# Optimization experiments

Hardware: AMD Instinct MI355X
Metric: run time of the kernel (lower is better)

The kernel has to match this reference:

```python
import jax, jax.numpy as jnp
import numpy as np

D, H, W, C = 24, 24, 16, 2        # image_dims + num_classes
THETA_ALPHA = 160.0               # bilateral spatial std
THETA_BETA = 3.0                  # bilateral intensity std
THETA_GAMMA = 3.0                 # spatial-only std
NUM_ITERATIONS = 5
N = D * H * W


def _gauss_kernel(feats):
    # Dense Gaussian kernel K_ij = exp(-0.5 * ||f_i - f_j||^2).
    # This is the exact filter that the permutohedral lattice approximates
    # (self-term included, matching the lattice splat/blur/slice behaviour).
    sq = jnp.sum(feats * feats, axis=-1)               # [N]
    d2 = sq[:, None] + sq[None, :] - 2.0 * feats @ feats.T
    return jnp.exp(-0.5 * jnp.maximum(d2, 0.0))        # [N, N]


def _positions():
    zz, yy, xx = jnp.meshgrid(jnp.arange(D), jnp.arange(H), jnp.arange(W), indexing='ij')
    return jnp.stack([zz, yy, xx], axis=-1).reshape(N, 3).astype(jnp.float32)


def setup_inputs() -> dict:
    key = jax.random.key(0)
    k1, k2 = jax.random.split(key)
    unaries = jax.random.normal(k1, (1, D, H, W, C), dtype=jnp.float32)
    rgb = jax.random.uniform(k2, (1, D, H, W, 1), dtype=jnp.float32)
    # learned params (build() initial values)
    spatial_ker_weights = jnp.array([1.41, 1.41], dtype=jnp.float32)
    bilateral_ker_weights = jnp.array([3.85, 3.85], dtype=jnp.float32)
    compatibility_matrix = jnp.eye(C, dtype=jnp.float32)
    return dict(unaries=unaries, rgb=rgb,
                spatial_ker_weights=spatial_ker_weights,
                bilateral_ker_weights=bilateral_ker_weights,
                compatibility_matrix=compatibility_matrix)


def reference(unaries, rgb, spatial_ker_weights, bilateral_ker_weights, compatibility_matrix):
    out_shape = unaries.shape
    u = unaries.reshape(N, C)                 # batch index 0 only, as in the TF code
    img = rgb.reshape(N, -1)
    pos = _positions()

    Ks = _gauss_kernel(pos / THETA_GAMMA)                                        # spatial kernel [N,N]
    Kb = _gauss_kernel(jnp.concatenate([pos / THETA_ALPHA, img / THETA_BETA], -1))  # bilateral kernel [N,N]

    # normalization = filter applied to all-ones (row sums)
    norm_s = jnp.sum(Ks, axis=-1, keepdims=True)   # [N,1]
    norm_b = jnp.sum(Kb, axis=-1, keepdims=True)   # [N,1]

    q = u
    for _ in range(NUM_ITERATIONS):
        spatial_out = (Ks @ q) / norm_s            # [N,C]
        bilateral_out = (Kb @ q) / norm_b          # [N,C]
        # diag(w_s) @ spatial.T + diag(w_b) @ bilateral.T  ==  per-class scaling
        message = spatial_out * spatial_ker_weights + bilateral_out * bilateral_ker_weights
        pairwise = message @ compatibility_matrix.T  # (compat @ msg.T).T
        q = u - pairwise
    return q.reshape(out_shape)
```

## Files before the change

### kernel.cpp

```cpp
#include <hip/hip_runtime.h>


#define DD 24
#define HH 24
#define WW 16
#define SLICE 384
#define NPTS 9216
#define NT 5
#define NPAIR 6
#define NPTOT 9
#define LOG2E 1.4426950408889634f
#define K3L   (LOG2E / 18.0f)
#define K160L (LOG2E / 51200.0f)
#define EXP2  __builtin_amdgcn_exp2f

static __device__ __forceinline__ int iabs(int a) { return a < 0 ? -a : a; }

__global__ __launch_bounds__(SLICE)
void k_pre(const float2* __restrict__ u2, const float* __restrict__ rgb,
           float2* __restrict__ tmp2, float* __restrict__ normS) {
    __shared__ float gk[32];
    __shared__ float2 sA[HH][WW + 1];
    __shared__ float2 sB[HH][WW + 1];
    const int z = blockIdx.x, p = blockIdx.y, t = threadIdx.x;
    const int y = t >> 4, x = t & 15;
    const int i = z * SLICE + t;

    const float kk = (p == 0) ? K3L : K160L;
    if (t < DD) gk[t] = EXP2(-(float)(t * t) * kk);

    const float I3 = rgb[i] * (1.f / 3.f);
    float Pt[NT];
    Pt[0] = EXP2(-0.5f * LOG2E * I3 * I3);
#pragma unroll
    for (int k = 1; k < NT; ++k) Pt[k] = Pt[k - 1] * I3;

    float2 v;
    if (p == 0) {
        v = u2[i];
    } else if (p < NPAIR) {
        float2 q = u2[i];
        float P = Pt[p - 1];
        v = make_float2(P * q.x, P * q.y);
    } else {
        int j = p - NPAIR;
        v = make_float2(Pt[2 * j], (j < 2) ? Pt[2 * j + 1] : 0.f);
    }
    sA[y][x] = v;
    __syncthreads();

    float a0 = 0.f, a1 = 0.f;
#pragma unroll
    for (int xp = 0; xp < WW; ++xp) {
        float w = gk[iabs(x - xp)];
        float2 vv = sA[y][xp];
        a0 = fmaf(w, vv.x, a0);
        a1 = fmaf(w, vv.y, a1);
    }
    sB[y][x] = make_float2(a0, a1);
    __syncthreads();
    float b0 = 0.f, b1 = 0.f;
#pragma unroll
    for (int yp = 0; yp < HH; ++yp) {
        float w = gk[iabs(y - yp)];
        float2 vv = sB[yp][x];
        b0 = fmaf(w, vv.x, b0);
        b1 = fmaf(w, vv.y, b1);
    }
    tmp2[p * NPTS + i] = make_float2(b0, b1);

    if (p == 0) {
        float sx = 0.f, sy = 0.f, sz = 0.f;
#pragma unroll
        for (int xp = 0; xp < WW; ++xp) sx += gk[iabs(x - xp)];
#pragma unroll
        for (int yp = 0; yp < HH; ++yp) sy += gk[iabs(y - yp)];
#pragma unroll
        for (int zp = 0; zp < DD; ++zp) sz += gk[iabs(z - zp)];
        normS[i] = 1.0f / (sx * sy * sz);
    }
}

__global__ __launch_bounds__(SLICE)
void k_zconv(const float2* __restrict__ tmp2, float2* __restrict__ zout2) {
    const int z = blockIdx.x, p = blockIdx.y, t = threadIdx.x;
    const float kk = (p == 0) ? K3L : K160L;
    float acc0 = 0.f, acc1 = 0.f;
    const float2* src = tmp2 + p * NPTS + t;
#pragma unroll 6
    for (int zp = 0; zp < DD; ++zp) {
        int d = z - zp;
        float w = EXP2(-(float)(d * d) * kk);
        float2 v = src[zp * SLICE];
        acc0 = fmaf(w, v.x, acc0);
        acc1 = fmaf(w, v.y, acc1);
    }
    zout2[p * NPTS + z * SLICE + t] = make_float2(acc0, acc1);
}

static __device__ __forceinline__ void mf_update(
        const float2 zp_[NPAIR], const float* Pt, float inv_ns, float inv_nb,
        const float* sw, const float* bw, const float* compat,
        const float2 uu, float* q0o, float* q1o) {
    const float invf[NT] = {1.f, 1.f, 0.5f, 1.f / 6.f, 1.f / 24.f};
    float b0 = 0.f, b1 = 0.f;
#pragma unroll
    for (int k = 0; k < NT; ++k) {
        float w = Pt[k] * invf[k];
        b0 = fmaf(w, zp_[1 + k].x, b0);
        b1 = fmaf(w, zp_[1 + k].y, b1);
    }
    b0 *= inv_nb;
    b1 *= inv_nb;
    float s0 = zp_[0].x * inv_ns;
    float s1 = zp_[0].y * inv_ns;
    float m0 = s0 * sw[0] + b0 * bw[0];
    float m1 = s1 * sw[1] + b1 * bw[1];
    float p0 = fmaf(compat[0], m0, compat[1] * m1);
    float p1 = fmaf(compat[2], m0, compat[3] * m1);
    *q0o = uu.x - p0;
    *q1o = uu.y - p1;
}

__global__ __launch_bounds__(SLICE)
void k_xyupd(const float2* __restrict__ zout2, const float* __restrict__ rgb,
             const float2* __restrict__ u2,
             const float* __restrict__ sw, const float* __restrict__ bw,
             const float* __restrict__ compat,
             const float* __restrict__ normS, float* __restrict__ normB,
             float2* __restrict__ tmp2, int it) {
    __shared__ float gk[32];
    __shared__ float2 sA[HH][WW + 1];
    __shared__ float2 sB[HH][WW + 1];
    const int z = blockIdx.x, p = blockIdx.y, t = threadIdx.x;
    const int y = t >> 4, x = t & 15;
    const int i = z * SLICE + t;

    const float kk = (p == 0) ? K3L : K160L;
    if (t < DD) gk[t] = EXP2(-(float)(t * t) * kk);

    float2 zp_[NPAIR];
#pragma unroll
    for (int k = 0; k < NPAIR; ++k) zp_[k] = zout2[k * NPTS + i];

    const float I3 = rgb[i] * (1.f / 3.f);
    float Pt[NT];
    Pt[0] = EXP2(-0.5f * LOG2E * I3 * I3);
#pragma unroll
    for (int k = 1; k < NT; ++k) Pt[k] = Pt[k - 1] * I3;

    float inv_nb;
    if (it == 0) {
        float2 n0 = zout2[6 * NPTS + i];
        float2 n1 = zout2[7 * NPTS + i];
        float2 n2 = zout2[8 * NPTS + i];
        float nb = Pt[0] * n0.x + Pt[1] * n0.y + 0.5f * Pt[2] * n1.x
                 + (1.f / 6.f) * Pt[3] * n1.y + (1.f / 24.f) * Pt[4] * n2.x;
        if (p == 0) normB[i] = nb;
        inv_nb = 1.0f / nb;
    } else {
        inv_nb = 1.0f / normB[i];
    }

    float q0, q1;
    mf_update(zp_, Pt, normS[i], inv_nb, sw, bw, compat, u2[i], &q0, &q1);

    float2 v;
    if (p == 0) v = make_float2(q0, q1);
    else { float P = Pt[p - 1]; v = make_float2(P * q0, P * q1); }

    sA[y][x] = v;
    __syncthreads();
    float a0 = 0.f, a1 = 0.f;
#pragma unroll
    for (int xp = 0; xp < WW; ++xp) {
        float w = gk[iabs(x - xp)];
        float2 vv = sA[y][xp];
        a0 = fmaf(w, vv.x, a0);
        a1 = fmaf(w, vv.y, a1);
    }
    sB[y][x] = make_float2(a0, a1);
    __syncthreads();
    float b0 = 0.f, b1 = 0.f;
#pragma unroll
    for (int yp = 0; yp < HH; ++yp) {
        float w = gk[iabs(y - yp)];
        float2 vv = sB[yp][x];
        b0 = fmaf(w, vv.x, b0);
        b1 = fmaf(w, vv.y, b1);
    }
    tmp2[p * NPTS + i] = make_float2(b0, b1);
}

__global__ __launch_bounds__(256)
void k_final(const float2* __restrict__ zout2, const float* __restrict__ rgb,
             const float2* __restrict__ u2,
             const float* __restrict__ sw, const float* __restrict__ bw,
             const float* __restrict__ compat,
             const float* __restrict__ normS, const float* __restrict__ normB,
             float2* __restrict__ out) {
    const int i = blockIdx.x * 256 + threadIdx.x;

    float2 zp_[NPAIR];
#pragma unroll
    for (int k = 0; k < NPAIR; ++k) zp_[k] = zout2[k * NPTS + i];

    const float I3 = rgb[i] * (1.f / 3.f);
    float Pt[NT];
    Pt[0] = EXP2(-0.5f * LOG2E * I3 * I3);
#pragma unroll
    for (int k = 1; k < NT; ++k) Pt[k] = Pt[k - 1] * I3;

    float q0, q1;
    mf_update(zp_, Pt, normS[i], 1.0f / normB[i], sw, bw, compat,
              u2[i], &q0, &q1);
    out[i] = make_float2(q0, q1);
}

extern "C" void kernel_launch(void* const* d_in, const int* in_sizes, int n_in,
                              void* d_out, int out_size, void* d_ws, size_t ws_size,
                              hipStream_t stream) {
    const float2* u2     = (const float2*)d_in[0];
    const float*  rgb    = (const float*)d_in[1];
    const float*  sw     = (const float*)d_in[2];
    const float*  bw     = (const float*)d_in[3];
    const float*  compat = (const float*)d_in[4];
    float2* out = (float2*)d_out;

    float2* ws2   = (float2*)d_ws;
    float2* tmp2  = ws2;
    float2* zout2 = ws2 + NPTOT * NPTS;
    float*  normS = (float*)(ws2 + 2 * NPTOT * NPTS);
    float*  normB = normS + NPTS;

    k_pre<<<dim3(DD, NPTOT), SLICE, 0, stream>>>(u2, rgb, tmp2, normS);

    for (int it = 0; it < 5; ++it) {
        k_zconv<<<dim3(DD, it == 0 ? NPTOT : NPAIR), SLICE, 0, stream>>>(tmp2, zout2);
        if (it < 4)
            k_xyupd<<<dim3(DD, NPAIR), SLICE, 0, stream>>>(zout2, rgb, u2, sw, bw,
                                                           compat, normS, normB,
                                                           tmp2, it);
        else
            k_final<<<NPTS / 256, 256, 0, stream>>>(zout2, rgb, u2, sw, bw,
                                                    compat, normS, normB, out);
    }
}
```

Baseline: 97.28 us.

## Fuse all CRF stages into one persistent kernel with global barriers

```diff
diff --git a/kernel.cpp b/kernel.cpp
--- a/kernel.cpp
+++ b/kernel.cpp
@@ -8,7 +8,7 @@
 #define NPTS 9216
 #define NT 5
 #define NPAIR 6
-#define NPTOT 9
+#define NB (DD * NPAIR)
 #define LOG2E 1.4426950408889634f
 #define K3L   (LOG2E / 18.0f)
 #define K160L (LOG2E / 51200.0f)
@@ -16,39 +16,42 @@
 
 static __device__ __forceinline__ int iabs(int a) { return a < 0 ? -a : a; }
 
-__global__ __launch_bounds__(SLICE)
-void k_pre(const float2* __restrict__ u2, const float* __restrict__ rgb,
-           float2* __restrict__ tmp2, float* __restrict__ normS) {
-    __shared__ float gk[32];
-    __shared__ float2 sA[HH][WW + 1];
-    __shared__ float2 sB[HH][WW + 1];
-    const int z = blockIdx.x, p = blockIdx.y, t = threadIdx.x;
-    const int y = t >> 4, x = t & 15;
-    const int i = z * SLICE + t;
-
-    const float kk = (p == 0) ? K3L : K160L;
-    if (t < DD) gk[t] = EXP2(-(float)(t * t) * kk);
-
-    const float I3 = rgb[i] * (1.f / 3.f);
-    float Pt[NT];
-    Pt[0] = EXP2(-0.5f * LOG2E * I3 * I3);
-#pragma unroll
-    for (int k = 1; k < NT; ++k) Pt[k] = Pt[k - 1] * I3;
-
-    float2 v;
-    if (p == 0) {
-        v = u2[i];
-    } else if (p < NPAIR) {
-        float2 q = u2[i];
-        float P = Pt[p - 1];
-        v = make_float2(P * q.x, P * q.y);
-    } else {
-        int j = p - NPAIR;
-        v = make_float2(Pt[2 * j], (j < 2) ? Pt[2 * j + 1] : 0.f);
-    }
+static __device__ __forceinline__ float2 ldc2(const float2* p) {
+    unsigned long long v = __hip_atomic_load((unsigned long long*)p,
+                               __ATOMIC_RELAXED, __HIP_MEMORY_SCOPE_AGENT);
+    float2 f;
+    __builtin_memcpy(&f, &v, 8);
+    return f;
+}
+static __device__ __forceinline__ void stc2(float2* p, float2 f) {
+    unsigned long long v;
+    __builtin_memcpy(&v, &f, 8);
+    __hip_atomic_store((unsigned long long*)p, v,
+                       __ATOMIC_RELAXED, __HIP_MEMORY_SCOPE_AGENT);
+}
+
+static __device__ __forceinline__ void gbar(unsigned* bar, int ph) {
+    __syncthreads();
+    if (threadIdx.x == 0) {
+        __builtin_amdgcn_s_waitcnt(0);
+        __hip_atomic_fetch_add(&bar[ph], 1u, __ATOMIC_RELAXED,
+                               __HIP_MEMORY_SCOPE_AGENT);
+        while (__hip_atomic_load(&bar[ph], __ATOMIC_RELAXED,
+                                 __HIP_MEMORY_SCOPE_AGENT) < (unsigned)NB)
+            __builtin_amdgcn_s_sleep(2);
+    }
+    __syncthreads();
+}
+
+__global__ void k_init(unsigned* bar) {
+    if (threadIdx.x < 16) bar[threadIdx.x] = 0u;
+}
+
+static __device__ void xyconv(float2 v, int y, int x, const float* gk,
+                              float2 (*sA)[WW + 1], float2 (*sB)[WW + 1],
+                              float2* ov) {
     sA[y][x] = v;
     __syncthreads();
-
     float a0 = 0.f, a1 = 0.f;
 #pragma unroll
     for (int xp = 0; xp < WW; ++xp) {
@@ -67,154 +70,141 @@
         b0 = fmaf(w, vv.x, b0);
         b1 = fmaf(w, vv.y, b1);
     }
-    tmp2[p * NPTS + i] = make_float2(b0, b1);
-
-    if (p == 0) {
-        float sx = 0.f, sy = 0.f, sz = 0.f;
-#pragma unroll
-        for (int xp = 0; xp < WW; ++xp) sx += gk[iabs(x - xp)];
-#pragma unroll
-        for (int yp = 0; yp < HH; ++yp) sy += gk[iabs(y - yp)];
-#pragma unroll
-        for (int zp = 0; zp < DD; ++zp) sz += gk[iabs(z - zp)];
-        normS[i] = 1.0f / (sx * sy * sz);
-    }
-}
-
-__global__ __launch_bounds__(SLICE)
-void k_zconv(const float2* __restrict__ tmp2, float2* __restrict__ zout2) {
-    const int z = blockIdx.x, p = blockIdx.y, t = threadIdx.x;
-    const float kk = (p == 0) ? K3L : K160L;
-    float acc0 = 0.f, acc1 = 0.f;
-    const float2* src = tmp2 + p * NPTS + t;
-#pragma unroll 6
-    for (int zp = 0; zp < DD; ++zp) {
-        int d = z - zp;
-        float w = EXP2(-(float)(d * d) * kk);
-        float2 v = src[zp * SLICE];
-        acc0 = fmaf(w, v.x, acc0);
-        acc1 = fmaf(w, v.y, acc1);
-    }
-    zout2[p * NPTS + z * SLICE + t] = make_float2(acc0, acc1);
-}
-
-static __device__ __forceinline__ void mf_update(
-        const float2 zp_[NPAIR], const float* Pt, float inv_ns, float inv_nb,
-        const float* sw, const float* bw, const float* compat,
-        const float2 uu, float* q0o, float* q1o) {
-    const float invf[NT] = {1.f, 1.f, 0.5f, 1.f / 6.f, 1.f / 24.f};
-    float b0 = 0.f, b1 = 0.f;
-#pragma unroll
-    for (int k = 0; k < NT; ++k) {
-        float w = Pt[k] * invf[k];
-        b0 = fmaf(w, zp_[1 + k].x, b0);
-        b1 = fmaf(w, zp_[1 + k].y, b1);
-    }
-    b0 *= inv_nb;
-    b1 *= inv_nb;
-    float s0 = zp_[0].x * inv_ns;
-    float s1 = zp_[0].y * inv_ns;
-    float m0 = s0 * sw[0] + b0 * bw[0];
-    float m1 = s1 * sw[1] + b1 * bw[1];
-    float p0 = fmaf(compat[0], m0, compat[1] * m1);
-    float p1 = fmaf(compat[2], m0, compat[3] * m1);
-    *q0o = uu.x - p0;
-    *q1o = uu.y - p1;
-}
-
-__global__ __launch_bounds__(SLICE)
-void k_xyupd(const float2* __restrict__ zout2, const float* __restrict__ rgb,
-             const float2* __restrict__ u2,
-             const float* __restrict__ sw, const float* __restrict__ bw,
-             const float* __restrict__ compat,
-             const float* __restrict__ normS, float* __restrict__ normB,
-             float2* __restrict__ tmp2, int it) {
+    *ov = make_float2(b0, b1);
+    __syncthreads();
+}
+
+__global__ __launch_bounds__(SLICE, 1)
+void crf_fused(const float2* __restrict__ u2, const float* __restrict__ rgb,
+               const float* __restrict__ sw, const float* __restrict__ bw,
+               const float* __restrict__ compat,
+               float2* __restrict__ tmp, float2* __restrict__ tmpN,
+               float2* __restrict__ zout, float2* __restrict__ zoutN,
+               unsigned* __restrict__ bar, float2* __restrict__ out) {
     __shared__ float gk[32];
+    __shared__ float g3s[32];
     __shared__ float2 sA[HH][WW + 1];
     __shared__ float2 sB[HH][WW + 1];
+
     const int z = blockIdx.x, p = blockIdx.y, t = threadIdx.x;
     const int y = t >> 4, x = t & 15;
     const int i = z * SLICE + t;
 
     const float kk = (p == 0) ? K3L : K160L;
-    if (t < DD) gk[t] = EXP2(-(float)(t * t) * kk);
-
-    float2 zp_[NPAIR];
-#pragma unroll
-    for (int k = 0; k < NPAIR; ++k) zp_[k] = zout2[k * NPTS + i];
+    if (t < DD) {
+        gk[t] = EXP2(-(float)(t * t) * kk);
+        g3s[t] = EXP2(-(float)(t * t) * K3L);
+    }
+    __syncthreads();
 
     const float I3 = rgb[i] * (1.f / 3.f);
     float Pt[NT];
     Pt[0] = EXP2(-0.5f * LOG2E * I3 * I3);
 #pragma unroll
     for (int k = 1; k < NT; ++k) Pt[k] = Pt[k - 1] * I3;
-
-    float inv_nb;
-    if (it == 0) {
-        float2 n0 = zout2[6 * NPTS + i];
-        float2 n1 = zout2[7 * NPTS + i];
-        float2 n2 = zout2[8 * NPTS + i];
-        float nb = Pt[0] * n0.x + Pt[1] * n0.y + 0.5f * Pt[2] * n1.x
-                 + (1.f / 6.f) * Pt[3] * n1.y + (1.f / 24.f) * Pt[4] * n2.x;
-        if (p == 0) normB[i] = nb;
-        inv_nb = 1.0f / nb;
-    } else {
-        inv_nb = 1.0f / normB[i];
-    }
-
-    float q0, q1;
-    mf_update(zp_, Pt, normS[i], inv_nb, sw, bw, compat, u2[i], &q0, &q1);
-
-    float2 v;
-    if (p == 0) v = make_float2(q0, q1);
-    else { float P = Pt[p - 1]; v = make_float2(P * q0, P * q1); }
-
-    sA[y][x] = v;
-    __syncthreads();
-    float a0 = 0.f, a1 = 0.f;
-#pragma unroll
-    for (int xp = 0; xp < WW; ++xp) {
-        float w = gk[iabs(x - xp)];
-        float2 vv = sA[y][xp];
-        a0 = fmaf(w, vv.x, a0);
-        a1 = fmaf(w, vv.y, a1);
-    }
-    sB[y][x] = make_float2(a0, a1);
-    __syncthreads();
-    float b0 = 0.f, b1 = 0.f;
-#pragma unroll
-    for (int yp = 0; yp < HH; ++yp) {
-        float w = gk[iabs(y - yp)];
-        float2 vv = sB[yp][x];
-        b0 = fmaf(w, vv.x, b0);
-        b1 = fmaf(w, vv.y, b1);
-    }
-    tmp2[p * NPTS + i] = make_float2(b0, b1);
-}
-
-__global__ __launch_bounds__(256)
-void k_final(const float2* __restrict__ zout2, const float* __restrict__ rgb,
-             const float2* __restrict__ u2,
-             const float* __restrict__ sw, const float* __restrict__ bw,
-             const float* __restrict__ compat,
-             const float* __restrict__ normS, const float* __restrict__ normB,
-             float2* __restrict__ out) {
-    const int i = blockIdx.x * 256 + threadIdx.x;
-
-    float2 zp_[NPAIR];
-#pragma unroll
-    for (int k = 0; k < NPAIR; ++k) zp_[k] = zout2[k * NPTS + i];
-
-    const float I3 = rgb[i] * (1.f / 3.f);
-    float Pt[NT];
-    Pt[0] = EXP2(-0.5f * LOG2E * I3 * I3);
-#pragma unroll
-    for (int k = 1; k < NT; ++k) Pt[k] = Pt[k - 1] * I3;
-
-    float q0, q1;
-    mf_update(zp_, Pt, normS[i], 1.0f / normB[i], sw, bw, compat,
-              u2[i], &q0, &q1);
-    out[i] = make_float2(q0, q1);
+    const float2 uu = u2[i];
+    const float sw0 = sw[0], sw1 = sw[1];
+    const float bw0 = bw[0], bw1 = bw[1];
+    const float c00 = compat[0], c01 = compat[1];
+    const float c10 = compat[2], c11 = compat[3];
+
+    float sx = 0.f, sy = 0.f, sz = 0.f;
+#pragma unroll
+    for (int xp = 0; xp < WW; ++xp) sx += g3s[iabs(x - xp)];
+#pragma unroll
+    for (int yp = 0; yp < HH; ++yp) sy += g3s[iabs(y - yp)];
+#pragma unroll
+    for (int zp = 0; zp < DD; ++zp) sz += g3s[iabs(z - zp)];
+    const float inv_ns = 1.0f / (sx * sy * sz);
+    const float invf[NT] = {1.f, 1.f, 0.5f, 1.f / 6.f, 1.f / 24.f};
+
+    {
+        float2 v, ov;
+        if (p == 0) v = uu;
+        else { float P = Pt[p - 1]; v = make_float2(P * uu.x, P * uu.y); }
+        xyconv(v, y, x, gk, sA, sB, &ov);
+        stc2(&tmp[p * NPTS + i], ov);
+        if (p >= 1 && p <= 3) {
+            int j = p - 1;
+            float2 nv = make_float2(Pt[2 * j], (j < 2) ? Pt[2 * j + 1] : 0.f);
+            xyconv(nv, y, x, gk, sA, sB, &ov);
+            stc2(&tmpN[j * NPTS + i], ov);
+        }
+    }
+    gbar(bar, 0);
+
+    float inv_nb = 0.f;
+    for (int it = 0; it < 5; ++it) {
+        {
+            float a0 = 0.f, a1 = 0.f;
+            const float2* src = tmp + p * NPTS + t;
+            for (int zp = 0; zp < DD; ++zp) {
+                int d = z - zp;
+                float w = EXP2(-(float)(d * d) * kk);
+                float2 vv = ldc2(&src[zp * SLICE]);
+                a0 = fmaf(w, vv.x, a0);
+                a1 = fmaf(w, vv.y, a1);
+            }
+            stc2(&zout[p * NPTS + z * SLICE + t], make_float2(a0, a1));
+        }
+        if (it == 0 && p >= 1 && p <= 3) {
+            int j = p - 1;
+            float a0 = 0.f, a1 = 0.f;
+            const float2* src = tmpN + j * NPTS + t;
+            for (int zp = 0; zp < DD; ++zp) {
+                int d = z - zp;
+                float w = EXP2(-(float)(d * d) * K160L);
+                float2 vv = ldc2(&src[zp * SLICE]);
+                a0 = fmaf(w, vv.x, a0);
+                a1 = fmaf(w, vv.y, a1);
+            }
+            stc2(&zoutN[j * NPTS + z * SLICE + t], make_float2(a0, a1));
+        }
+        gbar(bar, 1 + 2 * it);
+
+        float2 zp_[NPAIR];
+#pragma unroll
+        for (int k = 0; k < NPAIR; ++k) zp_[k] = ldc2(&zout[k * NPTS + i]);
+
+        if (it == 0) {
+            float2 n0 = ldc2(&zoutN[0 * NPTS + i]);
+            float2 n1 = ldc2(&zoutN[1 * NPTS + i]);
+            float2 n2 = ldc2(&zoutN[2 * NPTS + i]);
+            float nb = Pt[0] * n0.x + Pt[1] * n0.y + 0.5f * Pt[2] * n1.x
+                     + (1.f / 6.f) * Pt[3] * n1.y + (1.f / 24.f) * Pt[4] * n2.x;
+            inv_nb = 1.0f / nb;
+        }
+
+        float b0 = 0.f, b1 = 0.f;
+#pragma unroll
+        for (int k = 0; k < NT; ++k) {
+            float w = Pt[k] * invf[k];
+            b0 = fmaf(w, zp_[1 + k].x, b0);
+            b1 = fmaf(w, zp_[1 + k].y, b1);
+        }
+        b0 *= inv_nb;
+        b1 *= inv_nb;
+        float s0 = zp_[0].x * inv_ns;
+        float s1 = zp_[0].y * inv_ns;
+        float m0 = s0 * sw0 + b0 * bw0;
+        float m1 = s1 * sw1 + b1 * bw1;
+        float p0 = fmaf(c00, m0, c01 * m1);
+        float p1 = fmaf(c10, m0, c11 * m1);
+        float q0 = uu.x - p0;
+        float q1 = uu.y - p1;
+
+        if (it == 4) {
+            if (p == 0) out[i] = make_float2(q0, q1);
+            break;
+        }
+
+        float2 v, ov;
+        if (p == 0) v = make_float2(q0, q1);
+        else { float P = Pt[p - 1]; v = make_float2(P * q0, P * q1); }
+        xyconv(v, y, x, gk, sA, sB, &ov);
+        stc2(&tmp[p * NPTS + i], ov);
+        gbar(bar, 2 + 2 * it);
+    }
 }
 
 extern "C" void kernel_launch(void* const* d_in, const int* in_sizes, int n_in,
@@ -228,21 +218,14 @@
     float2* out = (float2*)d_out;
 
     float2* ws2   = (float2*)d_ws;
-    float2* tmp2  = ws2;
-    float2* zout2 = ws2 + NPTOT * NPTS;
-    float*  normS = (float*)(ws2 + 2 * NPTOT * NPTS);
-    float*  normB = normS + NPTS;
-
-    k_pre<<<dim3(DD, NPTOT), SLICE, 0, stream>>>(u2, rgb, tmp2, normS);
-
-    for (int it = 0; it < 5; ++it) {
-        k_zconv<<<dim3(DD, it == 0 ? NPTOT : NPAIR), SLICE, 0, stream>>>(tmp2, zout2);
-        if (it < 4)
-            k_xyupd<<<dim3(DD, NPAIR), SLICE, 0, stream>>>(zout2, rgb, u2, sw, bw,
-                                                           compat, normS, normB,
-                                                           tmp2, it);
-        else
-            k_final<<<NPTS / 256, 256, 0, stream>>>(zout2, rgb, u2, sw, bw,
-                                                    compat, normS, normB, out);
-    }
-}
+    float2* tmp   = ws2;
+    float2* tmpN  = ws2 + 6 * NPTS;
+    float2* zout  = ws2 + 9 * NPTS;
+    float2* zoutN = ws2 + 15 * NPTS;
+    unsigned* bar = (unsigned*)(ws2 + 18 * NPTS);
+
+    k_init<<<1, 64, 0, stream>>>(bar);
+    crf_fused<<<dim3(DD, NPAIR), SLICE, 0, stream>>>(u2, rgb, sw, bw, compat,
+                                                     tmp, tmpN, zout, zoutN,
+                                                     bar, out);
+}
```

Result: slower. 144.2 us (+48.2%).
